# Performance work log

Measured on AMD Instinct MI355X. Metric: run time of the kernel, lower is better.

## Reference

```python
import jax, jax.numpy as jnp
import numpy as np

H = 128      # hidden_channels
NB = 128     # num_bilinear (must equal H per original code's scatter buffer)
NSR = 42     # num_spherical * num_radial = 7 * 6
E = 250000   # num edges
T = 1000000  # num triplets


def setup_inputs() -> dict:
    key = jax.random.key(0)
    ks = jax.random.split(key, 20)

    def lin(k, fan_in, fan_out):
        return jax.random.normal(k, (fan_in, fan_out), jnp.float32) / np.sqrt(fan_in)

    inp = {
        "x": jax.random.normal(ks[0], (E, H), jnp.float32),
        "rbf": jax.random.normal(ks[1], (E, H), jnp.float32),
        "sbf": jax.random.normal(ks[2], (T, NSR), jnp.float32),
        "idx_kj": jax.random.randint(ks[3], (T,), 0, E),
        "idx_ji": jax.random.randint(ks[4], (T,), 0, E),
        # lin_rbf2
        "W_rbf2": lin(ks[5], H, H), "b_rbf2": jnp.zeros((H,), jnp.float32),
        # lin_sbf1 / lin_sbf2 (no bias)
        "W_sbf1": lin(ks[6], NSR, NB),
        "W_sbf2": lin(ks[7], NB, NB),
        # lin_kj
        "W_kj": lin(ks[8], H, H), "b_kj": jnp.zeros((H,), jnp.float32),
        # down / up projections
        "W_down": lin(ks[9], H, NB), "b_down": jnp.zeros((NB,), jnp.float32),
        "W_up": lin(ks[10], NB, H), "b_up": jnp.zeros((H,), jnp.float32),
        # one ResidualLayer (num_before_skip = 1)
        "W_r1a": lin(ks[11], H, H), "b_r1a": jnp.zeros((H,), jnp.float32),
        "W_r1b": lin(ks[12], H, H), "b_r1b": jnp.zeros((H,), jnp.float32),
    }
    return inp


def reference(x, rbf, sbf, idx_kj, idx_ji,
              W_rbf2, b_rbf2, W_sbf1, W_sbf2, W_kj, b_kj,
              W_down, b_down, W_up, b_up,
              W_r1a, b_r1a, W_r1b, b_r1b):
    act = jax.nn.silu  # swish

    x_ji = x
    x_kj = act(x @ W_kj + b_kj)                      # [E, H]
    rbf_t = act(rbf @ W_rbf2 + b_rbf2)               # [E, H]
    x_kj = x_kj * rbf_t
    x_kj = act(x_kj @ W_down + b_down)               # [E, NB]
    x_kj = x_kj[idx_kj]                              # gather -> [T, NB]
    s = act(act(sbf @ W_sbf1) @ W_sbf2)              # [T, NB]
    x_kj = x_kj * s
    x_kj = act(x_kj @ W_up + b_up)                   # [T, H]
    # scatter-add into per-edge buffer (original index_add_ into zeros)
    m = jax.ops.segment_sum(x_kj, idx_ji, num_segments=x.shape[0])  # [E, H]
    # ResidualLayer (num_before_skip = 1)
    m = m + act(act(m @ W_r1a + b_r1a) @ W_r1b + b_r1b)
    return m + x_ji
```

## Files before the change

kernel.cpp:

```cpp
#include <hip/hip_runtime.h>
#include <hip/hip_bf16.h>


#define HD 128

typedef short  short8 __attribute__((ext_vector_type(8)));
typedef __bf16 bf16x8 __attribute__((ext_vector_type(8)));
typedef float  f32x4  __attribute__((ext_vector_type(4)));

__device__ __forceinline__ float b2f(short s) {
    unsigned u = ((unsigned)(unsigned short)s) << 16;
    return __builtin_bit_cast(float, u);
}
__device__ __forceinline__ short f2b(float f) {
    return __builtin_bit_cast(short, __float2bfloat16(f));
}
__device__ __forceinline__ float silu_f(float v) {
    return v * __builtin_amdgcn_rcpf(1.0f + __expf(-v));
}
__device__ __forceinline__ short8 ld8(const short* p) { return *(const short8*)p; }

__device__ __forceinline__ f32x4 mfma16(short8 a, short8 b, f32x4 c) {
    return __builtin_amdgcn_mfma_f32_16x16x32_bf16(
        __builtin_bit_cast(bf16x8, a), __builtin_bit_cast(bf16x8, b), c, 0, 0, 0);
}

__device__ __forceinline__ short8 ld8f(const float* p) {
    f32x4 v0 = *(const f32x4*)p;
    f32x4 v1 = *(const f32x4*)(p + 4);
    short8 r;
#pragma unroll
    for (int j = 0; j < 4; j++) { r[j] = f2b(v0[j]); r[4 + j] = f2b(v1[j]); }
    return r;
}

__device__ void pack_weight(const float* __restrict__ W, int Kact, int KC,
                            short* frag, int tid, int nth) {
    int total = 8 * KC * 64;
    for (int e = tid; e < total; e += nth) {
        int lane = e & 63;
        int slot = e >> 6;
        int ct = slot / KC;
        int kc = slot - ct * KC;
        int n  = ct * 16 + (lane & 15);
        int kb = kc * 32 + (lane >> 4) * 8;
        short8 v;
#pragma unroll
        for (int j = 0; j < 8; j++) {
            int k = kb + j;
            v[j] = (k < Kact) ? f2b(W[k * HD + n]) : (short)0;
        }
        *(short8*)&frag[(slot * 64 + lane) * 8] = v;
    }
}

template <int KC>
__device__ __forceinline__ void gemm8(const short8* a, const short* fragW,
                                      int lane, f32x4* acc) {
#pragma unroll
    for (int kc = 0; kc < KC; kc++) {
#pragma unroll
        for (int ct = 0; ct < 8; ct++) {
            short8 b = ld8(&fragW[((ct * KC + kc) * 64 + lane) * 8]);
            acc[ct] = mfma16(a[kc], b, acc[ct]);
        }
    }
}

#define RT_S 136

extern "C" __global__ __launch_bounds__(896)
void kA(const float* __restrict__ x, const float* __restrict__ rbf,
        const float* __restrict__ Wkj, const float* __restrict__ bkj,
        const float* __restrict__ Wrbf2, const float* __restrict__ brbf2,
        const float* __restrict__ Wdown, const float* __restrict__ bdown,
        short* __restrict__ e_down, int ntiles) {
    extern __shared__ short smem[];
    short* fW1 = smem;
    short* fW2 = fW1 + 16384;
    short* fW3 = fW2 + 16384;
    short* rt0 = fW3 + 16384;
    int tid = threadIdx.x;
    pack_weight(Wkj,   HD, 4, fW1, tid, 896);
    pack_weight(Wrbf2, HD, 4, fW2, tid, 896);
    pack_weight(Wdown, HD, 4, fW3, tid, 896);
    __syncthreads();
    int lane = tid & 63, wave = tid >> 6;
    int m = lane & 15, q = lane >> 4;
    short* rt = rt0 + wave * (16 * RT_S);

    for (int tile = blockIdx.x * 14 + wave; tile < ntiles; tile += gridDim.x * 14) {
        long rowbase = (long)tile * 16;
        const float* xr = x   + (rowbase + m) * HD;
        const float* rr = rbf + (rowbase + m) * HD;
        short8 ax[4], ar[4];
#pragma unroll
        for (int kc = 0; kc < 4; kc++) {
            ax[kc] = ld8f(xr + kc * 32 + q * 8);
            ar[kc] = ld8f(rr + kc * 32 + q * 8);
        }
        f32x4 acc1[8], acc2[8];
#pragma unroll
        for (int ct = 0; ct < 8; ct++) { acc1[ct] = (f32x4){0,0,0,0}; acc2[ct] = (f32x4){0,0,0,0}; }
#pragma unroll
        for (int kc = 0; kc < 4; kc++) {
#pragma unroll
            for (int ct = 0; ct < 8; ct++) {
                acc1[ct] = mfma16(ax[kc], ld8(&fW1[((ct*4+kc)*64 + lane)*8]), acc1[ct]);
                acc2[ct] = mfma16(ar[kc], ld8(&fW2[((ct*4+kc)*64 + lane)*8]), acc2[ct]);
            }
        }
#pragma unroll
        for (int ct = 0; ct < 8; ct++) {
            int col = ct * 16 + m;
            float bk = bkj[col];
            float br = brbf2[col];
#pragma unroll
            for (int r = 0; r < 4; r++) {
                float h = silu_f(acc1[ct][r] + bk) * silu_f(acc2[ct][r] + br);
                rt[(q*4 + r) * RT_S + col] = f2b(h);
            }
        }
        short8 ah[4];
#pragma unroll
        for (int kc = 0; kc < 4; kc++) ah[kc] = ld8(&rt[m * RT_S + kc * 32 + q * 8]);
        f32x4 acc3[8];
#pragma unroll
        for (int ct = 0; ct < 8; ct++) acc3[ct] = (f32x4){0,0,0,0};
        gemm8<4>(ah, fW3, lane, acc3);
#pragma unroll
        for (int ct = 0; ct < 8; ct++) {
            int col = ct * 16 + m;
            float bd = bdown[col];
#pragma unroll
            for (int r = 0; r < 4; r++)
                rt[(q*4 + r) * RT_S + col] = f2b(silu_f(acc3[ct][r] + bd));
        }
        short* eg = e_down + (rowbase + m) * HD;
#pragma unroll
        for (int kc = 0; kc < 4; kc++)
            *(short8*)(eg + kc * 32 + q * 8) = ld8(&rt[m * RT_S + kc * 32 + q * 8]);
    }
}

extern "C" __global__ __launch_bounds__(1024)
void kB(const float* __restrict__ sbf, const int* __restrict__ idx_kj,
        const int* __restrict__ idx_ji,
        const float* __restrict__ W1, const float* __restrict__ W2,
        const float* __restrict__ Wup, const float* __restrict__ bup,
        const short* __restrict__ e_down, float* __restrict__ mb, int ntiles) {
    extern __shared__ short smem[];
    short* f1  = smem;
    short* f2  = f1 + 8192;
    short* f3  = f2 + 16384;
    short* rt0 = f3 + 16384;
    int tid = threadIdx.x;
    pack_weight(W1, 42, 2, f1, tid, 1024);
    pack_weight(W2, HD, 4, f2, tid, 1024);
    pack_weight(Wup, HD, 4, f3, tid, 1024);
    __syncthreads();
    int lane = tid & 63, wave = tid >> 6;
    int m = lane & 15, q = lane >> 4;
    short* rt = rt0 + wave * (16 * RT_S);
    short* st = rt;
    int* sti = (int*)st;
    const float2* sg2 = (const float2*)sbf;

    for (int tile = blockIdx.x * 16 + wave; tile < ntiles; tile += gridDim.x * 16) {
        long rowbase = (long)tile * 16;
#pragma unroll
        for (int i = 0; i < 9; i++) sti[lane + i * 64] = 0;
#pragma unroll
        for (int i = lane; i < 336; i += 64) {
            int r = i / 21, d = i - r * 21;
            float2 v = sg2[(rowbase + r) * 21 + d];
            st[r * 72 + d * 2]     = f2b(v.x);
            st[r * 72 + d * 2 + 1] = f2b(v.y);
        }
        short8 a0[2];
        a0[0] = ld8(&st[m * 72 + q * 8]);
        a0[1] = ld8(&st[m * 72 + 32 + q * 8]);
        f32x4 acc[8];
#pragma unroll
        for (int ct = 0; ct < 8; ct++) acc[ct] = (f32x4){0,0,0,0};
        gemm8<2>(a0, f1, lane, acc);
#pragma unroll
        for (int ct = 0; ct < 8; ct++) {
            int col = ct * 16 + m;
#pragma unroll
            for (int r = 0; r < 4; r++)
                rt[(q*4 + r) * RT_S + col] = f2b(silu_f(acc[ct][r]));
        }
        short8 a1[4];
#pragma unroll
        for (int kc = 0; kc < 4; kc++) a1[kc] = ld8(&rt[m * RT_S + kc * 32 + q * 8]);
#pragma unroll
        for (int ct = 0; ct < 8; ct++) acc[ct] = (f32x4){0,0,0,0};
        gemm8<4>(a1, f2, lane, acc);
#pragma unroll
        for (int ct = 0; ct < 8; ct++) {
            int col = ct * 16 + m;
#pragma unroll
            for (int r = 0; r < 4; r++)
                rt[(q*4 + r) * RT_S + col] = f2b(silu_f(acc[ct][r]));
        }
        int ikj = idx_kj[rowbase + m];
        const short* ep = e_down + (long)ikj * HD;
        short8 p[4];
#pragma unroll
        for (int kc = 0; kc < 4; kc++) {
            short8 ek = ld8(ep + kc * 32 + q * 8);
            short8 ss = ld8(&rt[m * RT_S + kc * 32 + q * 8]);
            short8 pr;
#pragma unroll
            for (int j = 0; j < 8; j++) pr[j] = f2b(b2f(ss[j]) * b2f(ek[j]));
            p[kc] = pr;
        }
        f32x4 acc3[8];
#pragma unroll
        for (int ct = 0; ct < 8; ct++) acc3[ct] = (f32x4){0,0,0,0};
        gemm8<4>(p, f3, lane, acc3);
        int jr[4];
#pragma unroll
        for (int r = 0; r < 4; r++) jr[r] = idx_ji[rowbase + q * 4 + r];
#pragma unroll
        for (int ct = 0; ct < 8; ct++) {
            int col = ct * 16 + m;
            float bu = bup[col];
#pragma unroll
            for (int r = 0; r < 4; r++) {
                float t = silu_f(acc3[ct][r] + bu);
                unsafeAtomicAdd(&mb[(long)jr[r] * HD + col], t);
            }
        }
    }
}

extern "C" __global__ __launch_bounds__(1024)
void kC(const float* __restrict__ mb, const float* __restrict__ x,
        const float* __restrict__ Wa, const float* __restrict__ ba,
        const float* __restrict__ Wb, const float* __restrict__ bb2,
        float* __restrict__ out, int ntiles) {
    extern __shared__ short smem[];
    short* f1  = smem;
    short* f2  = f1 + 16384;
    short* rt0 = f2 + 16384;
    int tid = threadIdx.x;
    pack_weight(Wa, HD, 4, f1, tid, 1024);
    pack_weight(Wb, HD, 4, f2, tid, 1024);
    __syncthreads();
    int lane = tid & 63, wave = tid >> 6;
    int m = lane & 15, q = lane >> 4;
    short* rt = rt0 + wave * (16 * RT_S);

    for (int tile = blockIdx.x * 16 + wave; tile < ntiles; tile += gridDim.x * 16) {
        long rowbase = (long)tile * 16;
        const float* mr = mb + (rowbase + m) * HD;
        short8 am[4];
#pragma unroll
        for (int kc = 0; kc < 4; kc++) am[kc] = ld8f(mr + kc * 32 + q * 8);
        f32x4 acc[8];
#pragma unroll
        for (int ct = 0; ct < 8; ct++) acc[ct] = (f32x4){0,0,0,0};
        gemm8<4>(am, f1, lane, acc);
#pragma unroll
        for (int ct = 0; ct < 8; ct++) {
            int col = ct * 16 + m;
            float bav = ba[col];
#pragma unroll
            for (int r = 0; r < 4; r++)
                rt[(q*4 + r) * RT_S + col] = f2b(silu_f(acc[ct][r] + bav));
        }
        short8 ah[4];
#pragma unroll
        for (int kc = 0; kc < 4; kc++) ah[kc] = ld8(&rt[m * RT_S + kc * 32 + q * 8]);
#pragma unroll
        for (int ct = 0; ct < 8; ct++) acc[ct] = (f32x4){0,0,0,0};
        gemm8<4>(ah, f2, lane, acc);
#pragma unroll
        for (int ct = 0; ct < 8; ct++) {
            int col = ct * 16 + m;
            float bbv = bb2[col];
#pragma unroll
            for (int r = 0; r < 4; r++) {
                long grow = rowbase + q * 4 + r;
                out[grow * HD + col] = mb[grow * HD + col]
                                     + silu_f(acc[ct][r] + bbv)
                                     + x[grow * HD + col];
            }
        }
    }
}

extern "C" void kernel_launch(void* const* d_in, const int* in_sizes, int n_in,
                              void* d_out, int out_size, void* d_ws, size_t ws_size,
                              hipStream_t stream) {
    const float* x      = (const float*)d_in[0];
    const float* rbf    = (const float*)d_in[1];
    const float* sbf    = (const float*)d_in[2];
    const int*   idx_kj = (const int*)d_in[3];
    const int*   idx_ji = (const int*)d_in[4];
    const float* W_rbf2 = (const float*)d_in[5];
    const float* b_rbf2 = (const float*)d_in[6];
    const float* W_sbf1 = (const float*)d_in[7];
    const float* W_sbf2 = (const float*)d_in[8];
    const float* W_kj   = (const float*)d_in[9];
    const float* b_kj   = (const float*)d_in[10];
    const float* W_down = (const float*)d_in[11];
    const float* b_down = (const float*)d_in[12];
    const float* W_up   = (const float*)d_in[13];
    const float* b_up   = (const float*)d_in[14];
    const float* W_r1a  = (const float*)d_in[15];
    const float* b_r1a  = (const float*)d_in[16];
    const float* W_r1b  = (const float*)d_in[17];
    const float* b_r1b  = (const float*)d_in[18];

    int E = in_sizes[0] / HD;
    int T = in_sizes[3];

    short* e_down = (short*)d_ws;
    float* mb = (float*)((char*)d_ws + (size_t)E * HD * 2);
    hipMemsetAsync(mb, 0, (size_t)E * HD * 4, stream);

    int ntA = E / 16;
    int ntB = T / 16;
    size_t ldsA = (size_t)(3 * 16384 + 14 * 16 * RT_S) * 2;
    size_t ldsB = (size_t)(8192 + 16384 + 16384 + 16 * 16 * RT_S) * 2;
    size_t ldsC = (size_t)(2 * 16384 + 16 * 16 * RT_S) * 2;

    kA<<<256, 896, ldsA, stream>>>(x, rbf, W_kj, b_kj, W_rbf2, b_rbf2,
                                   W_down, b_down, e_down, ntA);
    kB<<<256, 1024, ldsB, stream>>>(sbf, idx_kj, idx_ji, W_sbf1, W_sbf2,
                                    W_up, b_up, e_down, mb, ntB);
    kC<<<256, 1024, ldsC, stream>>>(mb, x, W_r1a, b_r1a, W_r1b, b_r1b,
                                    (float*)d_out, ntA);
}
```

Before: 1.027 ms.

## Sort triplets by destination edge and pre-reduce scatter atomics

Adds a counting-sort pass (histogram, three-stage scan, scatter) that groups triplet indices by idx_ji. The triplet kernel then processes triplets in sorted order, gathering sbf and idx_kj through the permutation and summing consecutive rows that share a destination before issuing each atomic, which cuts atomic traffic and makes it more local. The scatter buffer now lives in the output array, so kC reads and writes the same memory in place. The cost is five extra small launches, including a single-thread serial scan, plus gathered rather than streaming reads of sbf and idx_kj.

```diff
diff --git a/kernel.cpp b/kernel.cpp
--- a/kernel.cpp
+++ b/kernel.cpp
@@ -144,8 +144,66 @@
 }
 
 extern "C" __global__ __launch_bounds__(1024)
+void kHist(const int* __restrict__ idx_ji, int* __restrict__ counts, int T) {
+    for (int t = blockIdx.x * 1024 + threadIdx.x; t < T; t += gridDim.x * 1024)
+        atomicAdd(&counts[idx_ji[t]], 1);
+}
+
+extern "C" __global__ __launch_bounds__(1024)
+void kScan1(const int* __restrict__ counts, int* __restrict__ cursor,
+            int* __restrict__ bsum, int E) {
+    __shared__ int wpart[16];
+    int i = blockIdx.x * 1024 + threadIdx.x;
+    int lane = threadIdx.x & 63, wv = threadIdx.x >> 6;
+    int orig = (i < E) ? counts[i] : 0;
+    int v = orig;
+#pragma unroll
+    for (int d = 1; d < 64; d <<= 1) {
+        int n = __shfl_up(v, d);
+        if (lane >= d) v += n;
+    }
+    if (lane == 63) wpart[wv] = v;
+    __syncthreads();
+    if (wv == 0) {
+        int w = (lane < 16) ? wpart[lane] : 0;
+#pragma unroll
+        for (int d = 1; d < 16; d <<= 1) {
+            int n = __shfl_up(w, d);
+            if (lane >= d) w += n;
+        }
+        if (lane < 16) wpart[lane] = w;
+    }
+    __syncthreads();
+    int base = (wv > 0) ? wpart[wv - 1] : 0;
+    if (i < E) cursor[i] = base + v - orig;
+    if (threadIdx.x == 1023) bsum[blockIdx.x] = base + v;
+}
+
+extern "C" __global__ void kScan2(int* __restrict__ bsum, int nb) {
+    if (threadIdx.x == 0) {
+        int run = 0;
+        for (int b = 0; b < nb; b++) { int t = bsum[b]; bsum[b] = run; run += t; }
+    }
+}
+
+extern "C" __global__ __launch_bounds__(1024)
+void kScan3(int* __restrict__ cursor, const int* __restrict__ bsum, int E) {
+    int i = blockIdx.x * 1024 + threadIdx.x;
+    if (i < E) cursor[i] += bsum[blockIdx.x];
+}
+
+extern "C" __global__ __launch_bounds__(1024)
+void kScatter(const int* __restrict__ idx_ji, int* __restrict__ cursor,
+              int* __restrict__ trip, int T) {
+    for (int t = blockIdx.x * 1024 + threadIdx.x; t < T; t += gridDim.x * 1024) {
+        int p = atomicAdd(&cursor[idx_ji[t]], 1);
+        trip[p] = t;
+    }
+}
+
+extern "C" __global__ __launch_bounds__(1024)
 void kB(const float* __restrict__ sbf, const int* __restrict__ idx_kj,
-        const int* __restrict__ idx_ji,
+        const int* __restrict__ idx_ji, const int* __restrict__ trip,
         const float* __restrict__ W1, const float* __restrict__ W2,
         const float* __restrict__ Wup, const float* __restrict__ bup,
         const short* __restrict__ e_down, float* __restrict__ mb, int ntiles) {
@@ -168,12 +226,15 @@
 
     for (int tile = blockIdx.x * 16 + wave; tile < ntiles; tile += gridDim.x * 16) {
         long rowbase = (long)tile * 16;
+        int tr_l = trip[rowbase + m];
+        int ji_l = idx_ji[tr_l];
 #pragma unroll
         for (int i = 0; i < 9; i++) sti[lane + i * 64] = 0;
 #pragma unroll
         for (int i = lane; i < 336; i += 64) {
             int r = i / 21, d = i - r * 21;
-            float2 v = sg2[(rowbase + r) * 21 + d];
+            int trr = __shfl(tr_l, r);
+            float2 v = sg2[(long)trr * 21 + d];
             st[r * 72 + d * 2]     = f2b(v.x);
             st[r * 72 + d * 2 + 1] = f2b(v.y);
         }
@@ -204,7 +265,7 @@
             for (int r = 0; r < 4; r++)
                 rt[(q*4 + r) * RT_S + col] = f2b(silu_f(acc[ct][r]));
         }
-        int ikj = idx_kj[rowbase + m];
+        int ikj = idx_kj[tr_l];
         const short* ep = e_down + (long)ikj * HD;
         short8 p[4];
 #pragma unroll
@@ -220,27 +281,31 @@
 #pragma unroll
         for (int ct = 0; ct < 8; ct++) acc3[ct] = (f32x4){0,0,0,0};
         gemm8<4>(p, f3, lane, acc3);
-        int jr[4];
-#pragma unroll
-        for (int r = 0; r < 4; r++) jr[r] = idx_ji[rowbase + q * 4 + r];
+        int jb[4];
+#pragma unroll
+        for (int r = 0; r < 4; r++) jb[r] = __shfl(ji_l, q * 4 + r);
 #pragma unroll
         for (int ct = 0; ct < 8; ct++) {
             int col = ct * 16 + m;
             float bu = bup[col];
+            float run = 0.f;
 #pragma unroll
             for (int r = 0; r < 4; r++) {
-                float t = silu_f(acc3[ct][r] + bu);
-                unsafeAtomicAdd(&mb[(long)jr[r] * HD + col], t);
+                run += silu_f(acc3[ct][r] + bu);
+                if (r == 3 || jb[r] != jb[r + 1]) {
+                    unsafeAtomicAdd(&mb[(long)jb[r] * HD + col], run);
+                    run = 0.f;
+                }
             }
         }
     }
 }
 
 extern "C" __global__ __launch_bounds__(1024)
-void kC(const float* __restrict__ mb, const float* __restrict__ x,
+void kC(const float* mb, const float* __restrict__ x,
         const float* __restrict__ Wa, const float* __restrict__ ba,
         const float* __restrict__ Wb, const float* __restrict__ bb2,
-        float* __restrict__ out, int ntiles) {
+        float* out, int ntiles) {
     extern __shared__ short smem[];
     short* f1  = smem;
     short* f2  = f1 + 16384;
@@ -284,8 +349,8 @@
 #pragma unroll
             for (int r = 0; r < 4; r++) {
                 long grow = rowbase + q * 4 + r;
-                out[grow * HD + col] = mb[grow * HD + col]
-                                     + silu_f(acc[ct][r] + bbv)
+                float mv = mb[grow * HD + col];
+                out[grow * HD + col] = mv + silu_f(acc[ct][r] + bbv)
                                      + x[grow * HD + col];
             }
         }
@@ -319,18 +384,33 @@
     int T = in_sizes[3];
 
     short* e_down = (short*)d_ws;
-    float* mb = (float*)((char*)d_ws + (size_t)E * HD * 2);
+    char*  wp = (char*)d_ws + (size_t)E * HD * 2;
+    int* trip   = (int*)wp;  wp += (size_t)T * 4;
+    int* cursor = (int*)wp;  wp += (size_t)E * 4;
+    int* counts = (int*)wp;  wp += (size_t)E * 4;
+    int* bsum   = (int*)wp;
+
+    float* mb = (float*)d_out;
+
+    hipMemsetAsync(counts, 0, (size_t)E * 4, stream);
     hipMemsetAsync(mb, 0, (size_t)E * HD * 4, stream);
 
     int ntA = E / 16;
     int ntB = T / 16;
+    int nblkE = (E + 1023) / 1024;
     size_t ldsA = (size_t)(3 * 16384 + 14 * 16 * RT_S) * 2;
     size_t ldsB = (size_t)(8192 + 16384 + 16384 + 16 * 16 * RT_S) * 2;
     size_t ldsC = (size_t)(2 * 16384 + 16 * 16 * RT_S) * 2;
 
+    kHist   <<<512, 1024, 0, stream>>>(idx_ji, counts, T);
+    kScan1  <<<nblkE, 1024, 0, stream>>>(counts, cursor, bsum, E);
+    kScan2  <<<1, 64, 0, stream>>>(bsum, nblkE);
+    kScan3  <<<nblkE, 1024, 0, stream>>>(cursor, bsum, E);
+    kScatter<<<512, 1024, 0, stream>>>(idx_ji, cursor, trip, T);
+
     kA<<<256, 896, ldsA, stream>>>(x, rbf, W_kj, b_kj, W_rbf2, b_rbf2,
                                    W_down, b_down, e_down, ntA);
-    kB<<<256, 1024, ldsB, stream>>>(sbf, idx_kj, idx_ji, W_sbf1, W_sbf2,
+    kB<<<256, 1024, ldsB, stream>>>(sbf, idx_kj, idx_ji, trip, W_sbf1, W_sbf2,
                                     W_up, b_up, e_down, mb, ntB);
     kC<<<256, 1024, ldsC, stream>>>(mb, x, W_r1a, b_r1a, W_r1b, b_r1b,
                                     (float*)d_out, ntA);
```

After: 1.037 ms. About the same (+1.0%).
